# Kernel tuning notes

Measured on AMD Instinct MI355X. Metric: run time of the kernel, lower is better.

## Reference

```python
import jax, jax.numpy as jnp
import numpy as np

# hardcoded constants from Model.sample_regions / gather_regions / __init__
RADIUS = 0.4
REGIONS = 50
BALL_K = 1000
TOP_K = 4
NEIGHBORHOOD = 128
COURSE = 512


def square_distance(src, dst):
    """src [B,N,C], dst [B,M,C] -> squared dists [B,N,M]."""
    d = -2.0 * jnp.einsum('bnc,bmc->bnm', src, dst)
    d = d + jnp.sum(src * src, -1)[:, :, None]
    d = d + jnp.sum(dst * dst, -1)[:, None, :]
    return d


def furthest_point_sample(xyz, npoint):
    """xyz [B,N,3] -> indices [B,npoint] (deterministic start at point 0)."""
    B, N, _ = xyz.shape
    barange = jnp.arange(B)

    def body(carry, _):
        dist, last = carry                      # dist [B,N], last [B] int32
        centroid = xyz[barange, last]           # [B,3]
        d = jnp.sum((xyz - centroid[:, None, :]) ** 2, -1)
        dist = jnp.minimum(dist, d)
        nxt = jnp.argmax(dist, axis=-1).astype(jnp.int32)
        return (dist, nxt), last

    init = (jnp.full((B, N), 1e10, xyz.dtype), jnp.zeros((B,), jnp.int32))
    _, idxs = jax.lax.scan(body, init, None, length=npoint)
    return jnp.transpose(idxs)                  # [B, npoint]


def knn_point(k, xyz, new_xyz):
    """k-NN of new_xyz [B,S,3] among xyz [B,N,3] -> idx [B,S,k]."""
    d = square_distance(new_xyz, xyz)
    _, idx = jax.lax.top_k(-d, k)
    return idx


def gather_xyz(xyz, idx):
    """xyz [B,N,3], idx [B,S] -> [B,S,3]."""
    B = xyz.shape[0]
    return xyz[jnp.arange(B)[:, None], idx]


def gather_regions(p_xyz, a_xyz, radius):
    """p_xyz [B,N,3] points, a_xyz [B,A,3] anchors -> [B, TOP_K*NEIGHBORHOOD, 3]."""
    B = p_xyz.shape[0]
    d2 = square_distance(a_xyz, p_xyz)                       # [B,A,N]
    counts = jnp.minimum(jnp.sum(d2 < radius * radius, axis=2), BALL_K)
    _, topk_idx = jax.lax.top_k(counts, TOP_K)               # densest anchors [B,TOP_K]
    sel = gather_xyz(a_xyz, topk_idx)                        # [B,TOP_K,3]
    nidx = knn_point(NEIGHBORHOOD, p_xyz, sel)               # [B,TOP_K,NB]
    neigh = p_xyz[jnp.arange(B)[:, None, None], nidx]        # [B,TOP_K,NB,3]
    return neigh.reshape(B, TOP_K * NEIGHBORHOOD, 3)


def sample_regions(p_xyz, regions, r):
    anchors_idx = furthest_point_sample(p_xyz, regions)
    anchors = gather_xyz(p_xyz, anchors_idx)
    return gather_regions(p_xyz, anchors, r)


def setup_inputs() -> dict:
    key = jax.random.key(0)
    points = jax.random.normal(key, (16, 3, 16384), dtype=jnp.float32)
    return {"points": points}


def reference(points):
    # points [B,3,N] -> p_xyz [B,N,3]
    p_xyz = jnp.transpose(points, (0, 2, 1))
    roi1 = sample_regions(p_xyz, REGIONS, RADIUS)            # [B,512,3]
    roi2 = sample_regions(p_xyz, REGIONS, RADIUS)            # [B,512,3] (a == b == 0.4)
    fps_idx = furthest_point_sample(p_xyz, COURSE)           # [B,512]
    fps_pts = gather_xyz(p_xyz, fps_idx)                     # [B,512,3]
    return jnp.concatenate([roi1, roi2, fps_pts], axis=1)    # [B,1536,3]
```

## Files before the change

kernel.cpp:

```cpp
#include <hip/hip_runtime.h>
#include <stdint.h>

#define NPTS 16384
#define BATCH 16
#define FPS_N 512
#define NANCH 50
#define TOPK 4
#define NBH 128
#define BALLK 1000

#define FT 1024
#define NW 16

#define CTRL_XOR1 0xB1
#define CTRL_XOR2 0x4E
#define CTRL_ROR4 0x124
#define CTRL_ROR8 0x128

#define DPP_MAX64(v, CTRL) do {                                                   \
  unsigned int _lo = (unsigned int)(v);                                           \
  unsigned int _hi = (unsigned int)((v) >> 32);                                   \
  unsigned int _slo = (unsigned int)__builtin_amdgcn_update_dpp((int)_lo, (int)_lo, CTRL, 0xf, 0xf, false); \
  unsigned int _shi = (unsigned int)__builtin_amdgcn_update_dpp((int)_hi, (int)_hi, CTRL, 0xf, 0xf, false); \
  unsigned long long _o = (((unsigned long long)_shi) << 32) | _slo;              \
  if (_o > (v)) (v) = _o;                                                         \
} while (0)

#define DPP_MIN64(v, CTRL) do {                                                   \
  unsigned int _lo = (unsigned int)(v);                                           \
  unsigned int _hi = (unsigned int)((v) >> 32);                                   \
  unsigned int _slo = (unsigned int)__builtin_amdgcn_update_dpp((int)_lo, (int)_lo, CTRL, 0xf, 0xf, false); \
  unsigned int _shi = (unsigned int)__builtin_amdgcn_update_dpp((int)_hi, (int)_hi, CTRL, 0xf, 0xf, false); \
  unsigned long long _o = (((unsigned long long)_shi) << 32) | _slo;              \
  if (_o < (v)) (v) = _o;                                                         \
} while (0)

#define SWZ16_MIN64(v) do {                                                       \
  unsigned int _lo = (unsigned int)(v), _hi = (unsigned int)((v) >> 32);          \
  unsigned int _slo = (unsigned int)__builtin_amdgcn_ds_swizzle((int)_lo, 0x401f);\
  unsigned int _shi = (unsigned int)__builtin_amdgcn_ds_swizzle((int)_hi, 0x401f);\
  unsigned long long _o = (((unsigned long long)_shi) << 32) | _slo;              \
  if (_o < (v)) (v) = _o;                                                         \
} while (0)

#define SHF32_MIN64(v) do {                                                       \
  unsigned long long _o = __shfl_xor((v), 32, 64);                                \
  if (_o < (v)) (v) = _o;                                                         \
} while (0)

__device__ __forceinline__ uint32_t f2key(float f) {
  uint32_t u = __float_as_uint(f);
  return (u & 0x80000000u) ? ~u : (u | 0x80000000u);
}

#define REP8(OP) OP(0) OP(1) OP(2) OP(3) OP(4) OP(5) OP(6) OP(7)

__global__ __launch_bounds__(FT, 4) void mega_kernel(const float* __restrict__ pts,
                                                     float* __restrict__ out) {
  __shared__ unsigned long long s_key[2][NW];
  __shared__ float4 s_xyz[2][NW];
  __shared__ float4 s_anch[NANCH];
  __shared__ int s_cnt[NANCH];
  __shared__ int s_t4[TOPK];
  __shared__ int s_knn[NBH];

  const int bid = blockIdx.x;
  const bool isFps = bid < BATCH;
  const int b = isFps ? bid : ((bid - BATCH) >> 1);
  const int p = (bid - BATCH) & 1;
  const int nsteps = isFps ? FPS_N : NANCH;

  const int t = threadIdx.x;
  const int lane = t & 63;
  const int wS = t >> 6;
  const float* __restrict__ px = pts + (size_t)b * 3 * NPTS;
  const float* __restrict__ py = px + NPTS;
  const float* __restrict__ pz = py + NPTS;

#define DECLK(k) float2 x_##k, y_##k, z_##k, d_##k;
  REP8(DECLK)
#undef DECLK
#define LOADK(k) { const int i2 = ((k) << 11) + (t << 1);                  \
    x_##k = *(const float2*)&px[i2];                                       \
    y_##k = *(const float2*)&py[i2];                                       \
    z_##k = *(const float2*)&pz[i2];                                       \
    d_##k = make_float2(1e10f, 1e10f); }
  REP8(LOADK)
#undef LOADK
#define PINK(k) asm volatile("" : "+v"(x_##k), "+v"(y_##k), "+v"(z_##k));
  REP8(PINK)
#undef PINK

  float bx = px[0], by = py[0], bz = pz[0];
  if (t == 0) {
    if (isFps) {
      float* o = out + ((size_t)b * 1536 + 1024) * 3;
      o[0] = bx; o[1] = by; o[2] = bz;
    } else {
      s_anch[0] = make_float4(bx, by, bz, 0.f);
    }
  }

  for (int step = 1; step < nsteps; ++step) {
    const int par = step & 1;
    const float2 nbx2 = make_float2(-bx, -bx);
    const float2 nby2 = make_float2(-by, -by);
    const float2 nbz2 = make_float2(-bz, -bz);
    float run = -1.0f;
#define FPSK(k) {                                                          \
    float2 t0, t1, t2;                                                     \
    asm("v_pk_add_f32 %0, %3, %6\n\t"                                      \
        "v_pk_add_f32 %1, %4, %7\n\t"                                      \
        "v_pk_add_f32 %2, %5, %8\n\t"                                      \
        "v_pk_mul_f32 %0, %0, %0\n\t"                                      \
        "v_pk_mul_f32 %1, %1, %1\n\t"                                      \
        "v_pk_mul_f32 %2, %2, %2\n\t"                                      \
        "v_pk_add_f32 %0, %0, %1\n\t"                                      \
        "v_pk_add_f32 %0, %0, %2"                                          \
        : "=&v"(t0), "=&v"(t1), "=&v"(t2)                                  \
        : "v"(x_##k), "v"(y_##k), "v"(z_##k), "v"(nbx2), "v"(nby2), "v"(nbz2)); \
    d_##k.x = fminf(d_##k.x, t0.x);                                        \
    d_##k.y = fminf(d_##k.y, t0.y);                                        \
    asm("v_max3_f32 %0, %0, %1, %2"                                        \
        : "+v"(run) : "v"(d_##k.x), "v"(d_##k.y)); }
    REP8(FPSK)
#undef FPSK
    uint32_t m = __float_as_uint(run);
    {
      uint32_t s;
      s = (uint32_t)__builtin_amdgcn_update_dpp((int)m, (int)m, CTRL_XOR1, 0xf, 0xf, false); m = m > s ? m : s;
      s = (uint32_t)__builtin_amdgcn_update_dpp((int)m, (int)m, CTRL_XOR2, 0xf, 0xf, false); m = m > s ? m : s;
      s = (uint32_t)__builtin_amdgcn_update_dpp((int)m, (int)m, CTRL_ROR4, 0xf, 0xf, false); m = m > s ? m : s;
      s = (uint32_t)__builtin_amdgcn_update_dpp((int)m, (int)m, CTRL_ROR8, 0xf, 0xf, false); m = m > s ? m : s;
    }
    const uint32_t r0 = (uint32_t)__builtin_amdgcn_readlane((int)m, 0);
    const uint32_t r1 = (uint32_t)__builtin_amdgcn_readlane((int)m, 16);
    const uint32_t r2 = (uint32_t)__builtin_amdgcn_readlane((int)m, 32);
    const uint32_t r3 = (uint32_t)__builtin_amdgcn_readlane((int)m, 48);
    const uint32_t ra = r0 > r1 ? r0 : r1;
    const uint32_t rb = r2 > r3 ? r2 : r3;
    const uint32_t wm = ra > rb ? ra : rb;
    const float gmaxf = __uint_as_float(wm);
    uint32_t widx_w = 0u;
    bool done = false;
#define BALK(k) {                                                          \
    const unsigned long long b0 = __ballot(d_##k.x == gmaxf);              \
    const unsigned long long b1 = __ballot(d_##k.y == gmaxf);              \
    const unsigned long long cb = b0 | b1;                                 \
    if (!done && cb) {                                                     \
      const int l = (int)__builtin_ctzll(cb);                              \
      const uint32_t pp = ((b0 >> l) & 1ull) ? 0u : 1u;                    \
      widx_w = ((uint32_t)(k) << 11) + ((uint32_t)((wS << 6) | l) << 1) + pp; \
      if (lane == l) {                                                     \
        const float cx = pp ? x_##k.y : x_##k.x;                           \
        const float cy = pp ? y_##k.y : y_##k.x;                           \
        const float cz = pp ? z_##k.y : z_##k.x;                           \
        s_xyz[par][wS] = make_float4(cx, cy, cz, 0.f);                     \
      }                                                                    \
      done = true;                                                         \
    } }
    REP8(BALK)
#undef BALK
    if (lane == 0)
      s_key[par][wS] = ((unsigned long long)wm << 32) | (uint32_t)(~widx_w);
    __syncthreads();
    unsigned long long g = s_key[par][lane & 15];
    const float4 cand = s_xyz[par][lane & 15];
    DPP_MAX64(g, CTRL_XOR1);
    DPP_MAX64(g, CTRL_XOR2);
    DPP_MAX64(g, CTRL_ROR4);
    DPP_MAX64(g, CTRL_ROR8);
    const uint32_t widx = ~(uint32_t)g;
    const int wstar = (int)((widx >> 7) & 15);
    const int sw = __builtin_amdgcn_readfirstlane(wstar);
    bx = __uint_as_float((uint32_t)__builtin_amdgcn_readlane((int)__float_as_uint(cand.x), sw));
    by = __uint_as_float((uint32_t)__builtin_amdgcn_readlane((int)__float_as_uint(cand.y), sw));
    bz = __uint_as_float((uint32_t)__builtin_amdgcn_readlane((int)__float_as_uint(cand.z), sw));
    if (t == 0) {
      if (isFps) {
        float* o = out + ((size_t)b * 1536 + 1024 + step) * 3;
        o[0] = bx; o[1] = by; o[2] = bz;
      } else {
        s_anch[step] = make_float4(bx, by, bz, 0.f);
      }
    }
  }
  if (isFps) return;

#define DECLP(k) float2 p_##k;
  REP8(DECLP)
#undef DECLP
#define PSUMK(k) {                                                         \
    float2 s0, s1, s2;                                                     \
    asm("v_pk_mul_f32 %0, %3, %3\n\t"                                      \
        "v_pk_mul_f32 %1, %4, %4\n\t"                                      \
        "v_pk_mul_f32 %2, %5, %5\n\t"                                      \
        "v_pk_add_f32 %0, %0, %1\n\t"                                      \
        "v_pk_add_f32 %0, %0, %2"                                          \
        : "=&v"(s0), "=&v"(s1), "=&v"(s2)                                  \
        : "v"(x_##k), "v"(y_##k), "v"(z_##k));                             \
    p_##k = s0;                                                            \
    asm volatile("" : "+v"(p_##k)); }
  REP8(PSUMK)
#undef PSUMK
  if (t < NANCH) s_cnt[t] = 0;
  __syncthreads();

  const float R2 = (float)(0.4 * 0.4);
  const float2 mm2 = make_float2(-2.0f, -2.0f);
  for (int a = 0; a < NANCH; ++a) {
    const float4 A = s_anch[a];
    const float ax = A.x, ay = A.y, az = A.z;
    const float asum = __fadd_rn(__fadd_rn(__fmul_rn(ax, ax), __fmul_rn(ay, ay)),
                                 __fmul_rn(az, az));
    const float2 ax2 = make_float2(ax, ax);
    const float2 ay2 = make_float2(ay, ay);
    const float2 az2 = make_float2(az, az);
    const float2 as2 = make_float2(asum, asum);
    int cw = 0;
#define CNTK(k) {                                                          \
    float2 d0, d1, d2v;                                                    \
    asm("v_pk_mul_f32 %0, %3, %6\n\t"                                      \
        "v_pk_mul_f32 %1, %4, %7\n\t"                                      \
        "v_pk_mul_f32 %2, %5, %8\n\t"                                      \
        "v_pk_add_f32 %0, %0, %1\n\t"                                      \
        "v_pk_add_f32 %0, %0, %2\n\t"                                      \
        "v_pk_mul_f32 %0, %0, %9\n\t"                                      \
        "v_pk_add_f32 %0, %0, %10\n\t"                                     \
        "v_pk_add_f32 %0, %0, %11"                                         \
        : "=&v"(d0), "=&v"(d1), "=&v"(d2v)                                 \
        : "v"(x_##k), "v"(y_##k), "v"(z_##k), "v"(ax2), "v"(ay2), "v"(az2),\
          "v"(mm2), "v"(as2), "v"(p_##k));                                 \
    cw += (int)__popcll(__ballot(d0.x < R2));                              \
    cw += (int)__popcll(__ballot(d0.y < R2)); }
    REP8(CNTK)
#undef CNTK
    if (lane == 0) atomicAdd(&s_cnt[a], cw);
  }
  __syncthreads();

  if (t == 0) {
    unsigned long long used = 0ULL;
    for (int r = 0; r < TOPK; ++r) {
      int bestc = -1, besta = 0;
      for (int a = 0; a < NANCH; ++a) {
        if (used & (1ULL << a)) continue;
        int c = s_cnt[a];
        c = c < BALLK ? c : BALLK;
        if (c > bestc) { bestc = c; besta = a; }
      }
      used |= 1ULL << besta;
      s_t4[r] = besta;
    }
  }
  __syncthreads();

  for (int jj = 0; jj < 2; ++jj) {
    const int j = 2 * p + jj;
    const float4 A = s_anch[s_t4[j]];
    const float ax = A.x, ay = A.y, az = A.z;
    const float asum = __fadd_rn(__fadd_rn(__fmul_rn(ax, ax), __fmul_rn(ay, ay)),
                                 __fmul_rn(az, az));
    const float2 ax2 = make_float2(ax, ax);
    const float2 ay2 = make_float2(ay, ay);
    const float2 az2 = make_float2(az, az);
    const float2 as2 = make_float2(asum, asum);
#define DECLKK(k) unsigned long long ka_##k, kb_##k;
    REP8(DECLKK)
#undef DECLKK
#define KEYK(k) {                                                          \
    float2 d0, d1, d2v;                                                    \
    asm("v_pk_mul_f32 %0, %3, %6\n\t"                                      \
        "v_pk_mul_f32 %1, %4, %7\n\t"                                      \
        "v_pk_mul_f32 %2, %5, %8\n\t"                                      \
        "v_pk_add_f32 %0, %0, %1\n\t"                                      \
        "v_pk_add_f32 %0, %0, %2\n\t"                                      \
        "v_pk_mul_f32 %0, %0, %9\n\t"                                      \
        "v_pk_add_f32 %0, %0, %10\n\t"                                     \
        "v_pk_add_f32 %0, %0, %11"                                         \
        : "=&v"(d0), "=&v"(d1), "=&v"(d2v)                                 \
        : "v"(x_##k), "v"(y_##k), "v"(z_##k), "v"(ax2), "v"(ay2), "v"(az2),\
          "v"(mm2), "v"(as2), "v"(p_##k));                                 \
    const int i2 = ((k) << 11) + (t << 1);                                 \
    ka_##k = ((unsigned long long)f2key(d0.x) << 32) | (uint32_t)i2;       \
    kb_##k = ((unsigned long long)f2key(d0.y) << 32) | (uint32_t)(i2 + 1); }
    REP8(KEYK)
#undef KEYK
    for (int r = 0; r < NBH; ++r) {
#define PMINK(k) const unsigned long long w_##k = ka_##k < kb_##k ? ka_##k : kb_##k;
      REP8(PMINK)
#undef PMINK
      const unsigned long long q0 = w_0 < w_4 ? w_0 : w_4;
      const unsigned long long q1 = w_1 < w_5 ? w_1 : w_5;
      const unsigned long long q2 = w_2 < w_6 ? w_2 : w_6;
      const unsigned long long q3 = w_3 < w_7 ? w_3 : w_7;
      const unsigned long long r0m = q0 < q2 ? q0 : q2;
      const unsigned long long r1m = q1 < q3 ? q1 : q3;
      unsigned long long m = r0m < r1m ? r0m : r1m;

      DPP_MIN64(m, CTRL_XOR1);
      DPP_MIN64(m, CTRL_XOR2);
      DPP_MIN64(m, CTRL_ROR4);
      DPP_MIN64(m, CTRL_ROR8);
      SWZ16_MIN64(m);
      SHF32_MIN64(m);

      const int par = r & 1;
      if (lane == 0) s_key[par][wS] = m;
      __syncthreads();
      unsigned long long g = s_key[par][lane & 15];
      DPP_MIN64(g, CTRL_XOR1);
      DPP_MIN64(g, CTRL_XOR2);
      DPP_MIN64(g, CTRL_ROR4);
      DPP_MIN64(g, CTRL_ROR8);
      if (t == 0) s_knn[r] = (int)(uint32_t)g;
#define KILLK(k) { if (ka_##k == g) ka_##k = ~0ULL; if (kb_##k == g) kb_##k = ~0ULL; }
      REP8(KILLK)
#undef KILLK
    }
    __syncthreads();
    if (t < NBH) {
      const int idx = s_knn[t];
      const float X = px[idx], Y = py[idx], Z = pz[idx];
      float* o1 = out + ((size_t)b * 1536 + (j << 7) + t) * 3;
      float* o2 = o1 + 512 * 3;
      o1[0] = X; o1[1] = Y; o1[2] = Z;
      o2[0] = X; o2[1] = Y; o2[2] = Z;
    }
  }
}

extern "C" void kernel_launch(void* const* d_in, const int* in_sizes, int n_in,
                              void* d_out, int out_size, void* d_ws, size_t ws_size,
                              hipStream_t stream) {
  const float* pts = (const float*)d_in[0];
  float* out = (float*)d_out;
  (void)d_ws; (void)ws_size;
  mega_kernel<<<dim3(BATCH + 2 * BATCH), dim3(FT), 0, stream>>>(pts, out);
}
```

Before: 945.9 us.

## Shrink blocks to 256 threads with 64 points per thread in registers

Each block now runs 4 waves of 256 threads instead of 16 waves of 1024, and each thread holds 32 float2 groups (64 points) in registers instead of 8. Fewer waves mean the per-step cross-wave reductions through shared memory get cheaper, with shorter DPP chains and fewer participants at each barrier, which matters in the serial FPS and kNN loops. The cost is far more per-thread arithmetic and register pressure (launch bounds drop to 1 block per CU), so the 48 blocks expose much less parallelism per CU. A trailing barrier is added so the anchor loop does not race on shared memory between iterations.

```diff
diff --git a/kernel.cpp b/kernel.cpp
--- a/kernel.cpp
+++ b/kernel.cpp
@@ -9,8 +9,8 @@
 #define NBH 128
 #define BALLK 1000
 
-#define FT 1024
-#define NW 16
+#define FT 256
+#define NW 4
 
 #define CTRL_XOR1 0xB1
 #define CTRL_XOR2 0x4E
@@ -53,9 +53,12 @@
   return (u & 0x80000000u) ? ~u : (u | 0x80000000u);
 }
 
-#define REP8(OP) OP(0) OP(1) OP(2) OP(3) OP(4) OP(5) OP(6) OP(7)
-
-__global__ __launch_bounds__(FT, 4) void mega_kernel(const float* __restrict__ pts,
+#define REP32(OP) OP(0) OP(1) OP(2) OP(3) OP(4) OP(5) OP(6) OP(7) \
+  OP(8) OP(9) OP(10) OP(11) OP(12) OP(13) OP(14) OP(15) \
+  OP(16) OP(17) OP(18) OP(19) OP(20) OP(21) OP(22) OP(23) \
+  OP(24) OP(25) OP(26) OP(27) OP(28) OP(29) OP(30) OP(31)
+
+__global__ __launch_bounds__(FT, 1) void mega_kernel(const float* __restrict__ pts,
                                                      float* __restrict__ out) {
   __shared__ unsigned long long s_key[2][NW];
   __shared__ float4 s_xyz[2][NW];
@@ -78,17 +81,17 @@
   const float* __restrict__ pz = py + NPTS;
 
 #define DECLK(k) float2 x_##k, y_##k, z_##k, d_##k;
-  REP8(DECLK)
+  REP32(DECLK)
 #undef DECLK
-#define LOADK(k) { const int i2 = ((k) << 11) + (t << 1);                  \
+#define LOADK(k) { const int i2 = ((k) << 9) + (t << 1);                   \
     x_##k = *(const float2*)&px[i2];                                       \
     y_##k = *(const float2*)&py[i2];                                       \
     z_##k = *(const float2*)&pz[i2];                                       \
     d_##k = make_float2(1e10f, 1e10f); }
-  REP8(LOADK)
+  REP32(LOADK)
 #undef LOADK
 #define PINK(k) asm volatile("" : "+v"(x_##k), "+v"(y_##k), "+v"(z_##k));
-  REP8(PINK)
+  REP32(PINK)
 #undef PINK
 
   float bx = px[0], by = py[0], bz = pz[0];
@@ -123,7 +126,7 @@
     d_##k.y = fminf(d_##k.y, t0.y);                                        \
     asm("v_max3_f32 %0, %0, %1, %2"                                        \
         : "+v"(run) : "v"(d_##k.x), "v"(d_##k.y)); }
-    REP8(FPSK)
+    REP32(FPSK)
 #undef FPSK
     uint32_t m = __float_as_uint(run);
     {
@@ -150,7 +153,7 @@
     if (!done && cb) {                                                     \
       const int l = (int)__builtin_ctzll(cb);                              \
       const uint32_t pp = ((b0 >> l) & 1ull) ? 0u : 1u;                    \
-      widx_w = ((uint32_t)(k) << 11) + ((uint32_t)((wS << 6) | l) << 1) + pp; \
+      widx_w = ((uint32_t)(k) << 9) + ((uint32_t)((wS << 6) | l) << 1) + pp; \
       if (lane == l) {                                                     \
         const float cx = pp ? x_##k.y : x_##k.x;                           \
         const float cy = pp ? y_##k.y : y_##k.x;                           \
@@ -159,19 +162,17 @@
       }                                                                    \
       done = true;                                                         \
     } }
-    REP8(BALK)
+    REP32(BALK)
 #undef BALK
     if (lane == 0)
       s_key[par][wS] = ((unsigned long long)wm << 32) | (uint32_t)(~widx_w);
     __syncthreads();
-    unsigned long long g = s_key[par][lane & 15];
-    const float4 cand = s_xyz[par][lane & 15];
+    unsigned long long g = s_key[par][lane & 3];
+    const float4 cand = s_xyz[par][lane & 3];
     DPP_MAX64(g, CTRL_XOR1);
     DPP_MAX64(g, CTRL_XOR2);
-    DPP_MAX64(g, CTRL_ROR4);
-    DPP_MAX64(g, CTRL_ROR8);
     const uint32_t widx = ~(uint32_t)g;
-    const int wstar = (int)((widx >> 7) & 15);
+    const int wstar = (int)((widx >> 7) & 3);
     const int sw = __builtin_amdgcn_readfirstlane(wstar);
     bx = __uint_as_float((uint32_t)__builtin_amdgcn_readlane((int)__float_as_uint(cand.x), sw));
     by = __uint_as_float((uint32_t)__builtin_amdgcn_readlane((int)__float_as_uint(cand.y), sw));
@@ -188,7 +189,7 @@
   if (isFps) return;
 
 #define DECLP(k) float2 p_##k;
-  REP8(DECLP)
+  REP32(DECLP)
 #undef DECLP
 #define PSUMK(k) {                                                         \
     float2 s0, s1, s2;                                                     \
@@ -199,9 +200,8 @@
         "v_pk_add_f32 %0, %0, %2"                                          \
         : "=&v"(s0), "=&v"(s1), "=&v"(s2)                                  \
         : "v"(x_##k), "v"(y_##k), "v"(z_##k));                             \
-    p_##k = s0;                                                            \
-    asm volatile("" : "+v"(p_##k)); }
-  REP8(PSUMK)
+    p_##k = s0; }
+  REP32(PSUMK)
 #undef PSUMK
   if (t < NANCH) s_cnt[t] = 0;
   __syncthreads();
@@ -233,7 +233,7 @@
           "v"(mm2), "v"(as2), "v"(p_##k));                                 \
     cw += (int)__popcll(__ballot(d0.x < R2));                              \
     cw += (int)__popcll(__ballot(d0.y < R2)); }
-    REP8(CNTK)
+    REP32(CNTK)
 #undef CNTK
     if (lane == 0) atomicAdd(&s_cnt[a], cw);
   }
@@ -266,7 +266,7 @@
     const float2 az2 = make_float2(az, az);
     const float2 as2 = make_float2(asum, asum);
 #define DECLKK(k) unsigned long long ka_##k, kb_##k;
-    REP8(DECLKK)
+    REP32(DECLKK)
 #undef DECLKK
 #define KEYK(k) {                                                          \
     float2 d0, d1, d2v;                                                    \
@@ -281,19 +281,44 @@
         : "=&v"(d0), "=&v"(d1), "=&v"(d2v)                                 \
         : "v"(x_##k), "v"(y_##k), "v"(z_##k), "v"(ax2), "v"(ay2), "v"(az2),\
           "v"(mm2), "v"(as2), "v"(p_##k));                                 \
-    const int i2 = ((k) << 11) + (t << 1);                                 \
+    const int i2 = ((k) << 9) + (t << 1);                                  \
     ka_##k = ((unsigned long long)f2key(d0.x) << 32) | (uint32_t)i2;       \
     kb_##k = ((unsigned long long)f2key(d0.y) << 32) | (uint32_t)(i2 + 1); }
-    REP8(KEYK)
+    REP32(KEYK)
 #undef KEYK
     for (int r = 0; r < NBH; ++r) {
 #define PMINK(k) const unsigned long long w_##k = ka_##k < kb_##k ? ka_##k : kb_##k;
-      REP8(PMINK)
+      REP32(PMINK)
 #undef PMINK
-      const unsigned long long q0 = w_0 < w_4 ? w_0 : w_4;
-      const unsigned long long q1 = w_1 < w_5 ? w_1 : w_5;
-      const unsigned long long q2 = w_2 < w_6 ? w_2 : w_6;
-      const unsigned long long q3 = w_3 < w_7 ? w_3 : w_7;
+#define U16(k) const unsigned long long u_##k = w_##k < w_##k##_PLUS ? w_##k : w_##k##_PLUS;
+      const unsigned long long u0 = w_0 < w_16 ? w_0 : w_16;
+      const unsigned long long u1 = w_1 < w_17 ? w_1 : w_17;
+      const unsigned long long u2 = w_2 < w_18 ? w_2 : w_18;
+      const unsigned long long u3 = w_3 < w_19 ? w_3 : w_19;
+      const unsigned long long u4 = w_4 < w_20 ? w_4 : w_20;
+      const unsigned long long u5 = w_5 < w_21 ? w_5 : w_21;
+      const unsigned long long u6 = w_6 < w_22 ? w_6 : w_22;
+      const unsigned long long u7 = w_7 < w_23 ? w_7 : w_23;
+      const unsigned long long u8 = w_8 < w_24 ? w_8 : w_24;
+      const unsigned long long u9 = w_9 < w_25 ? w_9 : w_25;
+      const unsigned long long u10 = w_10 < w_26 ? w_10 : w_26;
+      const unsigned long long u11 = w_11 < w_27 ? w_11 : w_27;
+      const unsigned long long u12 = w_12 < w_28 ? w_12 : w_28;
+      const unsigned long long u13 = w_13 < w_29 ? w_13 : w_29;
+      const unsigned long long u14 = w_14 < w_30 ? w_14 : w_30;
+      const unsigned long long u15 = w_15 < w_31 ? w_15 : w_31;
+      const unsigned long long v0 = u0 < u8 ? u0 : u8;
+      const unsigned long long v1 = u1 < u9 ? u1 : u9;
+      const unsigned long long v2 = u2 < u10 ? u2 : u10;
+      const unsigned long long v3 = u3 < u11 ? u3 : u11;
+      const unsigned long long v4 = u4 < u12 ? u4 : u12;
+      const unsigned long long v5 = u5 < u13 ? u5 : u13;
+      const unsigned long long v6 = u6 < u14 ? u6 : u14;
+      const unsigned long long v7 = u7 < u15 ? u7 : u15;
+      const unsigned long long q0 = v0 < v4 ? v0 : v4;
+      const unsigned long long q1 = v1 < v5 ? v1 : v5;
+      const unsigned long long q2 = v2 < v6 ? v2 : v6;
+      const unsigned long long q3 = v3 < v7 ? v3 : v7;
       const unsigned long long r0m = q0 < q2 ? q0 : q2;
       const unsigned long long r1m = q1 < q3 ? q1 : q3;
       unsigned long long m = r0m < r1m ? r0m : r1m;
@@ -308,14 +333,12 @@
       const int par = r & 1;
       if (lane == 0) s_key[par][wS] = m;
       __syncthreads();
-      unsigned long long g = s_key[par][lane & 15];
+      unsigned long long g = s_key[par][lane & 3];
       DPP_MIN64(g, CTRL_XOR1);
       DPP_MIN64(g, CTRL_XOR2);
-      DPP_MIN64(g, CTRL_ROR4);
-      DPP_MIN64(g, CTRL_ROR8);
       if (t == 0) s_knn[r] = (int)(uint32_t)g;
 #define KILLK(k) { if (ka_##k == g) ka_##k = ~0ULL; if (kb_##k == g) kb_##k = ~0ULL; }
-      REP8(KILLK)
+      REP32(KILLK)
 #undef KILLK
     }
     __syncthreads();
@@ -327,6 +350,7 @@
       o1[0] = X; o1[1] = Y; o1[2] = Z;
       o2[0] = X; o2[1] = Y; o2[2] = Z;
     }
+    __syncthreads();
   }
 }
 
```

Result: slower. 1.809 ms (+91.2%).
